# Performance work log

Measured on AMD Instinct MI355X. Metric: run time of the kernel, lower is better.

The kernel has to match this reference:

```python
import jax, jax.numpy as jnp
import numpy as np

NUM_SCENES = 7
SHAPE = [512, 512, 256, 64]  # layer dims: 512->512->256->64
BATCH = 16384


def _xavier(key, shape):
    # nn.init.xavier_normal_ on (s, in, out): fan_in/fan_out from last two dims
    fan_in, fan_out = shape[-2], shape[-1]
    std = np.sqrt(2.0 / (fan_in + fan_out)).astype(np.float32)
    return jax.random.normal(key, shape, dtype=jnp.float32) * std


def setup_inputs() -> dict:
    key = jax.random.key(0)
    ks = jax.random.split(key, 16)
    inp = {
        "x": jax.random.normal(ks[0], (BATCH, SHAPE[0]), dtype=jnp.float32),
        "scene": jax.random.randint(ks[1], (BATCH,), 1, NUM_SCENES + 1, dtype=jnp.int64),
    }
    for i in range(3):
        din, dout = SHAPE[i], SHAPE[i + 1]
        inp[f"W{i}"] = _xavier(ks[2 + 4 * i], (NUM_SCENES, din, dout))
        inp[f"b{i}"] = jnp.zeros((NUM_SCENES, dout), dtype=jnp.float32)
        inp[f"gW{i}"] = _xavier(ks[3 + 4 * i], (1, din, dout))
        inp[f"gb{i}"] = jnp.zeros((1, dout), dtype=jnp.float32)
    return inp


def _star_linear(x, scene0, W, b, gW, gb, relu):
    # W: (S, in, out), gW: (1, in, out). Equivalent to gathering W[scene0]
    # and doing x[:,None,:] @ (w * gW), but computed as a dense GEMM over
    # all scenes followed by a per-sample select (avoids B*in*out gather).
    scaled = W * gW                                   # (S, in, out)
    out_all = jnp.einsum('bi,sio->bso', x, scaled)    # (B, S, out)
    out = jnp.take_along_axis(out_all, scene0[:, None, None], axis=1)[:, 0, :]
    out = out + b[scene0] + gb[0]
    if relu:
        out = jnp.maximum(out, 0.0)
    return out  # dropout is identity at eval


def reference(x, scene, W0, b0, gW0, gb0, W1, b1, gW1, gb1, W2, b2, gW2, gb2):
    scene0 = (scene - 1).astype(jnp.int32)
    h = _star_linear(x, scene0, W0, b0, gW0, gb0, relu=True)
    h = _star_linear(h, scene0, W1, b1, gW1, gb1, relu=True)
    h = _star_linear(h, scene0, W2, b2, gW2, gb2, relu=False)  # drop=True -> no relu
    return h
```

## Files before the change

### kernel.cpp

```cpp
#include <hip/hip_runtime.h>
#include <hip/hip_bf16.h>
#include <stdint.h>


#define BATCH   16384
#define NSCENE  7
#define TM      128
#define NBLK    (BATCH / 256)
#define MT_MAX  (BATCH / TM + NSCENE)
#define PADMAX  (BATCH + NSCENE * TM)

typedef __bf16 bf16x8 __attribute__((ext_vector_type(8)));
typedef float  f32x4  __attribute__((ext_vector_type(4)));

__device__ __forceinline__ ushort f2bf(float f) {
  union { float f; uint32_t u; } v; v.f = f;
  uint32_t r = (v.u + 0x7FFFu + ((v.u >> 16) & 1u)) >> 16;
  return (ushort)r;
}
__device__ __forceinline__ uint32_t pk2(float a, float b) {
  union { __hip_bfloat162 h; uint32_t u; } cv;
  cv.h = __float22bfloat162_rn(make_float2(a, b));
  return cv.u;
}
__device__ __forceinline__ void async16(const void* g, void* lds) {
  __builtin_amdgcn_global_load_lds(
      (const __attribute__((address_space(1))) uint32_t*)g,
      (__attribute__((address_space(3))) uint32_t*)lds, 16, 0, 0);
}

__device__ __forceinline__ void st_tile64(const float* __restrict__ W,
                                          const float* __restrict__ gW,
                                          ushort* __restrict__ sT,
                                          int K, int N, int s, int n0, int k0,
                                          int tid, float (*tl)[65]) {
  int tx = tid & 15, ty = tid >> 4;
  const float* Wp = W + (size_t)s * K * N;
#pragma unroll
  for (int i = 0; i < 4; i++) {
    int k = k0 + ty + i * 16;
    const float4 w = *(const float4*)&Wp[(size_t)k * N + n0 + tx * 4];
    const float4 g = *(const float4*)&gW[(size_t)k * N + n0 + tx * 4];
    float* row = &tl[ty + i * 16][tx * 4];
    row[0] = w.x * g.x; row[1] = w.y * g.y;
    row[2] = w.z * g.z; row[3] = w.w * g.w;
  }
  __syncthreads();
  int n_l = tid >> 2, kq = tid & 3;
  uint4 u0, u1;
  u0.x = pk2(tl[kq * 16 + 0][n_l],  tl[kq * 16 + 1][n_l]);
  u0.y = pk2(tl[kq * 16 + 2][n_l],  tl[kq * 16 + 3][n_l]);
  u0.z = pk2(tl[kq * 16 + 4][n_l],  tl[kq * 16 + 5][n_l]);
  u0.w = pk2(tl[kq * 16 + 6][n_l],  tl[kq * 16 + 7][n_l]);
  u1.x = pk2(tl[kq * 16 + 8][n_l],  tl[kq * 16 + 9][n_l]);
  u1.y = pk2(tl[kq * 16 + 10][n_l], tl[kq * 16 + 11][n_l]);
  u1.z = pk2(tl[kq * 16 + 12][n_l], tl[kq * 16 + 13][n_l]);
  u1.w = pk2(tl[kq * 16 + 14][n_l], tl[kq * 16 + 15][n_l]);
  uint4* dst = (uint4*)&sT[((size_t)s * N + n0 + n_l) * K + k0 + kq * 16];
  dst[0] = u0; dst[1] = u1;
}

#define NB_W0 (8 * 8 * 7)
#define NB_W1 (4 * 8 * 7)
#define NB_W2 (1 * 4 * 7)
#define NB_BIAS 23
#define NB_CNT NBLK

__global__ __launch_bounds__(256) void prep_k(
    const float* __restrict__ W0, const float* __restrict__ gW0,
    const float* __restrict__ W1, const float* __restrict__ gW1,
    const float* __restrict__ W2, const float* __restrict__ gW2,
    const float* __restrict__ b0, const float* __restrict__ gb0,
    const float* __restrict__ b1, const float* __restrict__ gb1,
    const float* __restrict__ b2, const float* __restrict__ gb2,
    const int* __restrict__ scene,
    ushort* __restrict__ sT0, ushort* __restrict__ sT1, ushort* __restrict__ sT2,
    float* __restrict__ bias0, float* __restrict__ bias1, float* __restrict__ bias2,
    int* __restrict__ bcnt, int* __restrict__ rank) {
  __shared__ float tl[64][65];
  int bid = blockIdx.x, tid = threadIdx.x;
  if (bid < NB_W0) {
    int l = bid, r = l % 64;
    st_tile64(W0, gW0, sT0, 512, 512, l / 64, (r % 8) * 64, (r / 8) * 64, tid, tl);
  } else if (bid < NB_W0 + NB_W1) {
    int l = bid - NB_W0, r = l % 32;
    st_tile64(W1, gW1, sT1, 512, 256, l / 32, (r % 4) * 64, (r / 4) * 64, tid, tl);
  } else if (bid < NB_W0 + NB_W1 + NB_W2) {
    int l = bid - NB_W0 - NB_W1;
    st_tile64(W2, gW2, sT2, 256, 64, l / 4, 0, (l % 4) * 64, tid, tl);
  } else if (bid < NB_W0 + NB_W1 + NB_W2 + NB_BIAS) {
    int t = (bid - NB_W0 - NB_W1 - NB_W2) * 256 + tid;
    if (t < 7 * 512) bias0[t] = b0[t] + gb0[t & 511];
    else if (t < 7 * 512 + 7 * 256) { int i = t - 7 * 512; bias1[i] = b1[i] + gb1[i & 255]; }
    else if (t < 7 * 512 + 7 * 256 + 7 * 64) { int i = t - 7 * 512 - 7 * 256; bias2[i] = b2[i] + gb2[i & 63]; }
  } else {
    __shared__ int l[NSCENE];
    if (tid < NSCENE) l[tid] = 0;
    __syncthreads();
    int blk = bid - NB_W0 - NB_W1 - NB_W2 - NB_BIAS;
    int i = blk * 256 + tid;
    int pos = atomicAdd(&l[scene[i] - 1], 1);
    rank[i] = pos;
    __syncthreads();
    if (tid < NSCENE) bcnt[blk * NSCENE + tid] = l[tid];
  }
}

__global__ __launch_bounds__(256) void xc_k(const float* __restrict__ x,
                                            const int* __restrict__ scene,
                                            const int* __restrict__ rank,
                                            const int* __restrict__ bcnt,
                                            int* __restrict__ idxp,
                                            ushort* __restrict__ xc,
                                            int* __restrict__ plan_g,
                                            float* __restrict__ out) {
  __shared__ int sb[NBLK * NSCENE];
  __shared__ int tot[NSCENE], padoff[NSCENE], cumt[NSCENE + 1];
  __shared__ int pre[NSCENE], base7[NSCENE];
  int tid = threadIdx.x;
  ((float2*)out)[(size_t)blockIdx.x * 256 + tid] = make_float2(0.f, 0.f);
  if (tid < NBLK * NSCENE) sb[tid] = bcnt[tid];
  if (tid + 256 < NBLK * NSCENE) sb[tid + 256] = bcnt[tid + 256];
  __syncthreads();
  int myblk = blockIdx.x >> 5;
  if (tid < 224) {
    int s = tid >> 5, l = tid & 31;
    int a0 = sb[l * NSCENE + s], a1 = sb[(l + 32) * NSCENE + s];
    int all = a0 + a1;
    int msk = (l < myblk ? a0 : 0) + (l + 32 < myblk ? a1 : 0);
#pragma unroll
    for (int m = 16; m >= 1; m >>= 1) {
      all += __shfl_xor(all, m, 32);
      msk += __shfl_xor(msk, m, 32);
    }
    if (l == 0) { tot[s] = all; pre[s] = msk; }
  }
  __syncthreads();
  if (tid == 0) {
    int po = 0, ct = 0;
#pragma unroll
    for (int s = 0; s < NSCENE; s++) {
      padoff[s] = po; cumt[s] = ct;
      int tiles = (tot[s] + TM - 1) / TM;
      ct += tiles; po += tiles * TM;
    }
    cumt[NSCENE] = ct;
  }
  __syncthreads();
  if (tid < NSCENE) base7[tid] = padoff[tid] + pre[tid];
  if (blockIdx.x == 0) {
    if (tid < NSCENE) { plan_g[tid] = tot[tid]; plan_g[7 + tid] = padoff[tid]; }
    if (tid < NSCENE + 1) plan_g[14 + tid] = cumt[tid];
  }
  __syncthreads();

  int r = blockIdx.x * 8 + (tid >> 5);
  int s = scene[r] - 1;
  int d = base7[s] + rank[r];
  if ((tid & 31) == 0) idxp[d] = r;
  int c = (tid & 31) * 16;
  const float4* p = (const float4*)(x + (size_t)r * 512 + c);
  float4 f0 = p[0], f1 = p[1], f2 = p[2], f3 = p[3];
  uint4 v0, v1;
  v0.x = pk2(f0.x, f0.y); v0.y = pk2(f0.z, f0.w);
  v0.z = pk2(f1.x, f1.y); v0.w = pk2(f1.z, f1.w);
  v1.x = pk2(f2.x, f2.y); v1.y = pk2(f2.z, f2.w);
  v1.z = pk2(f3.x, f3.y); v1.w = pk2(f3.z, f3.w);
  uint4* q = (uint4*)(xc + (size_t)d * 512 + c);
  q[0] = v0; q[1] = v1;
}

__global__ __launch_bounds__(256) void gemm0_k(
    const ushort* __restrict__ ain, const ushort* __restrict__ bw,
    const float* __restrict__ bias, const int* __restrict__ plan,
    ushort* __restrict__ hout) {
  __shared__ int splan[24];
  __shared__ __align__(16) ushort Abuf[64 * 64];
  __shared__ __align__(16) ushort Bbuf[128 * 64];

  int tid = threadIdx.x;
  if (tid < 22) splan[tid] = plan[tid];
  __syncthreads();
  const int* padoff = splan + 7;
  const int* cumt   = splan + 14;

  int j = blockIdx.x;
  int t = j >> 1;
  if (t >= cumt[NSCENE]) return;
  int sc = 0;
  while (sc < NSCENE - 1 && t >= cumt[sc + 1]) sc++;
  int mrow0 = padoff[sc] + (t - cumt[sc]) * TM + (j & 1) * 64;
  int nb = blockIdx.y;

  int lane = tid & 63, wid = tid >> 6;

  f32x4 acc[4][2];
#pragma unroll
  for (int mt = 0; mt < 4; mt++)
#pragma unroll
    for (int nt = 0; nt < 2; nt++) acc[mt][nt] = (f32x4){0.f, 0.f, 0.f, 0.f};

  const ushort* bwS = bw + ((size_t)sc * 512 + (size_t)nb * 128) * 512;

  for (int kb = 0; kb < 8; kb++) {
#pragma unroll
    for (int i = 0; i < 2; i++) {
      int c = tid + i * 256;
      int row = c >> 3, q = c & 7;
      int kg = q ^ (row & 7);
      async16(ain + (size_t)(mrow0 + row) * 512 + kb * 64 + kg * 8,
              &Abuf[(size_t)(i * 256 + wid * 64) * 8]);
    }
#pragma unroll
    for (int i = 0; i < 4; i++) {
      int c = tid + i * 256;
      int row = c >> 3, q = c & 7;
      int kg = q ^ (row & 7);
      async16(bwS + (size_t)row * 512 + kb * 64 + kg * 8,
              &Bbuf[(size_t)(i * 256 + wid * 64) * 8]);
    }
    __syncthreads();
#pragma unroll
    for (int kk = 0; kk < 64; kk += 32) {
      bf16x8 af[4], bfr[2];
      int kc = (kk >> 3) + (lane >> 4);
#pragma unroll
      for (int mt = 0; mt < 4; mt++) {
        int row = mt * 16 + (lane & 15);
        af[mt] = *(const bf16x8*)(&Abuf[(row * 8 + (kc ^ (row & 7))) * 8]);
      }
#pragma unroll
      for (int nt = 0; nt < 2; nt++) {
        int row = wid * 32 + nt * 16 + (lane & 15);
        bfr[nt] = *(const bf16x8*)(&Bbuf[(row * 8 + (kc ^ (row & 7))) * 8]);
      }
#pragma unroll
      for (int mt = 0; mt < 4; mt++)
#pragma unroll
        for (int nt = 0; nt < 2; nt++)
          acc[mt][nt] = __builtin_amdgcn_mfma_f32_16x16x32_bf16(af[mt], bfr[nt], acc[mt][nt], 0, 0, 0);
    }
    __syncthreads();
  }

#pragma unroll
  for (int mt = 0; mt < 4; mt++) {
    int rl0 = mt * 16 + (lane >> 4) * 4;
#pragma unroll
    for (int nt = 0; nt < 2; nt++) {
      int col = nb * 128 + wid * 32 + nt * 16 + (lane & 15);
      float bv = bias[sc * 512 + col];
#pragma unroll
      for (int r = 0; r < 4; r++) {
        float v = fmaxf(acc[mt][nt][r] + bv, 0.f);
        hout[(size_t)(mrow0 + rl0 + r) * 512 + col] = f2bf(v);
      }
    }
  }
}

__global__ __launch_bounds__(256) void gemm1_k(
    const ushort* __restrict__ hc1, const ushort* __restrict__ sT1,
    const ushort* __restrict__ sT2, const float* __restrict__ bias1,
    const float* __restrict__ bias2, const int* __restrict__ plan,
    const int* __restrict__ idxp, float* __restrict__ out) {
  __shared__ int splan[24];
  __shared__ __align__(16) ushort Abuf[64 * 64];
  __shared__ __align__(16) ushort Bbuf[128 * 64];
  __shared__ __align__(16) ushort h2[64 * 128];

  int tid = threadIdx.x;
  if (tid < 22) splan[tid] = plan[tid];
  __syncthreads();
  const int* tot    = splan;
  const int* padoff = splan + 7;
  const int* cumt   = splan + 14;

  int j = blockIdx.x;
  int t = j >> 1;
  if (t >= cumt[NSCENE]) return;
  int sc = 0;
  while (sc < NSCENE - 1 && t >= cumt[sc + 1]) sc++;
  int mrow0 = padoff[sc] + (t - cumt[sc]) * TM + (j & 1) * 64;
  int maxloc = padoff[sc] + tot[sc];
  if (mrow0 >= maxloc) return;
  int kr = blockIdx.y;

  int lane = tid & 63, wid = tid >> 6;

  f32x4 acc[4][2];
#pragma unroll
  for (int mt = 0; mt < 4; mt++)
#pragma unroll
    for (int nt = 0; nt < 2; nt++) acc[mt][nt] = (f32x4){0.f, 0.f, 0.f, 0.f};

  const ushort* b1p = sT1 + ((size_t)sc * 256 + (size_t)kr * 128) * 512;

  for (int kb = 0; kb < 8; kb++) {
#pragma unroll
    for (int i = 0; i < 2; i++) {
      int c = tid + i * 256;
      int row = c >> 3, q = c & 7;
      int kg = q ^ (row & 7);
      async16(hc1 + (size_t)(mrow0 + row) * 512 + kb * 64 + kg * 8,
              &Abuf[(size_t)(i * 256 + wid * 64) * 8]);
    }
#pragma unroll
    for (int i = 0; i < 4; i++) {
      int c = tid + i * 256;
      int row = c >> 3, q = c & 7;
      int kg = q ^ (row & 7);
      async16(b1p + (size_t)row * 512 + kb * 64 + kg * 8,
              &Bbuf[(size_t)(i * 256 + wid * 64) * 8]);
    }
    __syncthreads();
#pragma unroll
    for (int kk = 0; kk < 64; kk += 32) {
      bf16x8 af[4], bfr[2];
      int kc = (kk >> 3) + (lane >> 4);
#pragma unroll
      for (int mt = 0; mt < 4; mt++) {
        int row = mt * 16 + (lane & 15);
        af[mt] = *(const bf16x8*)(&Abuf[(row * 8 + (kc ^ (row & 7))) * 8]);
      }
#pragma unroll
      for (int nt = 0; nt < 2; nt++) {
        int row = wid * 32 + nt * 16 + (lane & 15);
        bfr[nt] = *(const bf16x8*)(&Bbuf[(row * 8 + (kc ^ (row & 7))) * 8]);
      }
#pragma unroll
      for (int mt = 0; mt < 4; mt++)
#pragma unroll
        for (int nt = 0; nt < 2; nt++)
          acc[mt][nt] = __builtin_amdgcn_mfma_f32_16x16x32_bf16(af[mt], bfr[nt], acc[mt][nt], 0, 0, 0);
    }
    __syncthreads();
  }

#pragma unroll
  for (int mt = 0; mt < 4; mt++) {
#pragma unroll
    for (int nt = 0; nt < 2; nt++) {
      int col = wid * 32 + nt * 16 + (lane & 15);
      float bv = bias1[sc * 256 + kr * 128 + col];
#pragma unroll
      for (int r = 0; r < 4; r++) {
        int row = mt * 16 + (lane >> 4) * 4 + r;
        float v = fmaxf(acc[mt][nt][r] + bv, 0.f);
        int cc = col >> 3;
        int cs = (cc & 8) | ((cc & 7) ^ (row & 7));
        h2[(row * 16 + cs) * 8 + (col & 7)] = f2bf(v);
      }
    }
  }
  __syncthreads();

  const ushort* b2p = sT2 + (size_t)sc * 64 * 256 + (size_t)kr * 128;
#pragma unroll
  for (int i = 0; i < 4; i++) {
    int p = tid + i * 256;
    int row = p >> 4, q = p & 15;
    int kg = (q & 8) | ((q & 7) ^ (row & 7));
    async16(b2p + (size_t)row * 256 + kg * 8,
            &Bbuf[(size_t)(i * 256 + wid * 64) * 8]);
  }
  __syncthreads();

  f32x4 acc2[4];
#pragma unroll
  for (int nt = 0; nt < 4; nt++) acc2[nt] = (f32x4){0.f, 0.f, 0.f, 0.f};

#pragma unroll
  for (int kk = 0; kk < 128; kk += 32) {
    int kc = (kk >> 3) + (lane >> 4);
    bf16x8 af;
    {
      int row = wid * 16 + (lane & 15);
      int ks = (kc & 8) | ((kc & 7) ^ (row & 7));
      af = *(const bf16x8*)(&h2[(row * 16 + ks) * 8]);
    }
    bf16x8 bfr[4];
#pragma unroll
    for (int nt = 0; nt < 4; nt++) {
      int n = nt * 16 + (lane & 15);
      int ks = (kc & 8) | ((kc & 7) ^ (n & 7));
      bfr[nt] = *(const bf16x8*)(&Bbuf[(n * 16 + ks) * 8]);
    }
#pragma unroll
    for (int nt = 0; nt < 4; nt++)
      acc2[nt] = __builtin_amdgcn_mfma_f32_16x16x32_bf16(af, bfr[nt], acc2[nt], 0, 0, 0);
  }

  int rowg[4], gidx[4];
#pragma unroll
  for (int r = 0; r < 4; r++) {
    rowg[r] = mrow0 + wid * 16 + (lane >> 4) * 4 + r;
    gidx[r] = idxp[rowg[r]];
  }
#pragma unroll
  for (int nt = 0; nt < 4; nt++) {
    int col = nt * 16 + (lane & 15);
    float bv = (kr == 0) ? bias2[sc * 64 + col] : 0.f;
#pragma unroll
    for (int r = 0; r < 4; r++) {
      if (rowg[r] < maxloc)
        atomicAdd(&out[(size_t)gidx[r] * 64 + col], acc2[nt][r] + bv);
    }
  }
}

extern "C" void kernel_launch(void* const* d_in, const int* in_sizes, int n_in,
                              void* d_out, int out_size, void* d_ws, size_t ws_size,
                              hipStream_t stream) {
  const float* x   = (const float*)d_in[0];
  const int* scene = (const int*)d_in[1];
  const float* W0  = (const float*)d_in[2];
  const float* b0  = (const float*)d_in[3];
  const float* gW0 = (const float*)d_in[4];
  const float* gb0 = (const float*)d_in[5];
  const float* W1  = (const float*)d_in[6];
  const float* b1  = (const float*)d_in[7];
  const float* gW1 = (const float*)d_in[8];
  const float* gb1 = (const float*)d_in[9];
  const float* W2  = (const float*)d_in[10];
  const float* b2  = (const float*)d_in[11];
  const float* gW2 = (const float*)d_in[12];
  const float* gb2 = (const float*)d_in[13];
  float* out = (float*)d_out;

  char* ws = (char*)d_ws;
  size_t off = 0;
  auto alloc = [&](size_t bytes) -> void* {
    void* p = ws + off;
    off = (off + bytes + 255) & ~(size_t)255;
    return p;
  };
  ushort* sT0   = (ushort*)alloc((size_t)7 * 512 * 512 * 2);
  ushort* sT1   = (ushort*)alloc((size_t)7 * 256 * 512 * 2);
  ushort* sT2   = (ushort*)alloc((size_t)7 * 64 * 256 * 2);
  float*  bias0 = (float*)alloc(7 * 512 * 4);
  float*  bias1 = (float*)alloc(7 * 256 * 4);
  float*  bias2 = (float*)alloc(7 * 64 * 4);
  int*    bcnt  = (int*)alloc(NBLK * NSCENE * 4);
  int*    rank  = (int*)alloc(BATCH * 4);
  int*    idxp  = (int*)alloc(PADMAX * 4);
  int*    plan  = (int*)alloc(32 * 4);
  ushort* xc    = (ushort*)alloc((size_t)PADMAX * 512 * 2);
  ushort* hc1   = (ushort*)alloc((size_t)PADMAX * 512 * 2);
  (void)ws_size; (void)n_in; (void)in_sizes; (void)out_size;

  prep_k<<<NB_W0 + NB_W1 + NB_W2 + NB_BIAS + NB_CNT, 256, 0, stream>>>(
      W0, gW0, W1, gW1, W2, gW2, b0, gb0, b1, gb1, b2, gb2, scene,
      sT0, sT1, sT2, bias0, bias1, bias2, bcnt, rank);
  xc_k<<<BATCH / 8, 256, 0, stream>>>(x, scene, rank, bcnt, idxp, xc, plan, out);

  gemm0_k<<<dim3(MT_MAX * 2, 4), 256, 0, stream>>>(xc, sT0, bias0, plan, hc1);
  gemm1_k<<<dim3(MT_MAX * 2, 2), 256, 0, stream>>>(hc1, sT1, sT2, bias1, bias2,
                                                   plan, idxp, out);
}
```

Measured before the change: 150.1 us.

## Split scene counting into its own kernel and fuse weight prep with x compaction

Scene counting moves out of the prep kernel into a small standalone count kernel. Weight scaling/transposition, bias merging and x compaction/bf16 conversion are merged into one launch. The weight-prep blocks and the x-compaction blocks now run concurrently instead of back to back, because only the counting has to come first. The kernel count stays the same, but the combined kernel uses more shared memory per block, which may reduce occupancy.

```diff
diff --git a/kernel.cpp b/kernel.cpp
--- a/kernel.cpp
+++ b/kernel.cpp
@@ -27,6 +27,20 @@
   __builtin_amdgcn_global_load_lds(
       (const __attribute__((address_space(1))) uint32_t*)g,
       (__attribute__((address_space(3))) uint32_t*)lds, 16, 0, 0);
+}
+
+__global__ __launch_bounds__(256) void count_k(const int* __restrict__ scene,
+                                               int* __restrict__ bcnt,
+                                               int* __restrict__ rank) {
+  __shared__ int l[NSCENE];
+  int tid = threadIdx.x, blk = blockIdx.x;
+  if (tid < NSCENE) l[tid] = 0;
+  __syncthreads();
+  int i = blk * 256 + tid;
+  int pos = atomicAdd(&l[scene[i] - 1], 1);
+  rank[i] = pos;
+  __syncthreads();
+  if (tid < NSCENE) bcnt[blk * NSCENE + tid] = l[tid];
 }
 
 __device__ __forceinline__ void st_tile64(const float* __restrict__ W,
@@ -64,65 +78,51 @@
 #define NB_W1 (4 * 8 * 7)
 #define NB_W2 (1 * 4 * 7)
 #define NB_BIAS 23
-#define NB_CNT NBLK
-
-__global__ __launch_bounds__(256) void prep_k(
+#define NB_XC  (BATCH / 8)
+
+__global__ __launch_bounds__(256) void prepxc_k(
     const float* __restrict__ W0, const float* __restrict__ gW0,
     const float* __restrict__ W1, const float* __restrict__ gW1,
     const float* __restrict__ W2, const float* __restrict__ gW2,
     const float* __restrict__ b0, const float* __restrict__ gb0,
     const float* __restrict__ b1, const float* __restrict__ gb1,
     const float* __restrict__ b2, const float* __restrict__ gb2,
-    const int* __restrict__ scene,
+    const float* __restrict__ x, const int* __restrict__ scene,
+    const int* __restrict__ rank, const int* __restrict__ bcnt,
     ushort* __restrict__ sT0, ushort* __restrict__ sT1, ushort* __restrict__ sT2,
     float* __restrict__ bias0, float* __restrict__ bias1, float* __restrict__ bias2,
-    int* __restrict__ bcnt, int* __restrict__ rank) {
+    int* __restrict__ idxp, ushort* __restrict__ xc,
+    int* __restrict__ plan_g, float* __restrict__ out) {
   __shared__ float tl[64][65];
+  __shared__ int sb[NBLK * NSCENE];
+  __shared__ int tot[NSCENE], padoff[NSCENE], cumt[NSCENE + 1];
+  __shared__ int pre[NSCENE], base7[NSCENE];
   int bid = blockIdx.x, tid = threadIdx.x;
   if (bid < NB_W0) {
     int l = bid, r = l % 64;
     st_tile64(W0, gW0, sT0, 512, 512, l / 64, (r % 8) * 64, (r / 8) * 64, tid, tl);
+    return;
   } else if (bid < NB_W0 + NB_W1) {
     int l = bid - NB_W0, r = l % 32;
     st_tile64(W1, gW1, sT1, 512, 256, l / 32, (r % 4) * 64, (r / 4) * 64, tid, tl);
+    return;
   } else if (bid < NB_W0 + NB_W1 + NB_W2) {
     int l = bid - NB_W0 - NB_W1;
     st_tile64(W2, gW2, sT2, 256, 64, l / 4, 0, (l % 4) * 64, tid, tl);
+    return;
   } else if (bid < NB_W0 + NB_W1 + NB_W2 + NB_BIAS) {
     int t = (bid - NB_W0 - NB_W1 - NB_W2) * 256 + tid;
     if (t < 7 * 512) bias0[t] = b0[t] + gb0[t & 511];
     else if (t < 7 * 512 + 7 * 256) { int i = t - 7 * 512; bias1[i] = b1[i] + gb1[i & 255]; }
     else if (t < 7 * 512 + 7 * 256 + 7 * 64) { int i = t - 7 * 512 - 7 * 256; bias2[i] = b2[i] + gb2[i & 63]; }
-  } else {
-    __shared__ int l[NSCENE];
-    if (tid < NSCENE) l[tid] = 0;
-    __syncthreads();
-    int blk = bid - NB_W0 - NB_W1 - NB_W2 - NB_BIAS;
-    int i = blk * 256 + tid;
-    int pos = atomicAdd(&l[scene[i] - 1], 1);
-    rank[i] = pos;
-    __syncthreads();
-    if (tid < NSCENE) bcnt[blk * NSCENE + tid] = l[tid];
-  }
-}
-
-__global__ __launch_bounds__(256) void xc_k(const float* __restrict__ x,
-                                            const int* __restrict__ scene,
-                                            const int* __restrict__ rank,
-                                            const int* __restrict__ bcnt,
-                                            int* __restrict__ idxp,
-                                            ushort* __restrict__ xc,
-                                            int* __restrict__ plan_g,
-                                            float* __restrict__ out) {
-  __shared__ int sb[NBLK * NSCENE];
-  __shared__ int tot[NSCENE], padoff[NSCENE], cumt[NSCENE + 1];
-  __shared__ int pre[NSCENE], base7[NSCENE];
-  int tid = threadIdx.x;
-  ((float2*)out)[(size_t)blockIdx.x * 256 + tid] = make_float2(0.f, 0.f);
+    return;
+  }
+  int xb = bid - (NB_W0 + NB_W1 + NB_W2 + NB_BIAS);
+  ((float2*)out)[(size_t)xb * 256 + tid] = make_float2(0.f, 0.f);
   if (tid < NBLK * NSCENE) sb[tid] = bcnt[tid];
   if (tid + 256 < NBLK * NSCENE) sb[tid + 256] = bcnt[tid + 256];
   __syncthreads();
-  int myblk = blockIdx.x >> 5;
+  int myblk = xb >> 5;
   if (tid < 224) {
     int s = tid >> 5, l = tid & 31;
     int a0 = sb[l * NSCENE + s], a1 = sb[(l + 32) * NSCENE + s];
@@ -148,13 +148,13 @@
   }
   __syncthreads();
   if (tid < NSCENE) base7[tid] = padoff[tid] + pre[tid];
-  if (blockIdx.x == 0) {
+  if (xb == 0) {
     if (tid < NSCENE) { plan_g[tid] = tot[tid]; plan_g[7 + tid] = padoff[tid]; }
     if (tid < NSCENE + 1) plan_g[14 + tid] = cumt[tid];
   }
   __syncthreads();
 
-  int r = blockIdx.x * 8 + (tid >> 5);
+  int r = xb * 8 + (tid >> 5);
   int s = scene[r] - 1;
   int d = base7[s] + rank[r];
   if ((tid & 31) == 0) idxp[d] = r;
@@ -449,10 +449,10 @@
   ushort* hc1   = (ushort*)alloc((size_t)PADMAX * 512 * 2);
   (void)ws_size; (void)n_in; (void)in_sizes; (void)out_size;
 
-  prep_k<<<NB_W0 + NB_W1 + NB_W2 + NB_BIAS + NB_CNT, 256, 0, stream>>>(
-      W0, gW0, W1, gW1, W2, gW2, b0, gb0, b1, gb1, b2, gb2, scene,
-      sT0, sT1, sT2, bias0, bias1, bias2, bcnt, rank);
-  xc_k<<<BATCH / 8, 256, 0, stream>>>(x, scene, rank, bcnt, idxp, xc, plan, out);
+  count_k<<<NBLK, 256, 0, stream>>>(scene, bcnt, rank);
+  prepxc_k<<<NB_W0 + NB_W1 + NB_W2 + NB_BIAS + NB_XC, 256, 0, stream>>>(
+      W0, gW0, W1, gW1, W2, gW2, b0, gb0, b1, gb1, b2, gb2, x, scene,
+      rank, bcnt, sT0, sT1, sT2, bias0, bias1, bias2, idxp, xc, plan, out);
 
   gemm0_k<<<dim3(MT_MAX * 2, 4), 256, 0, stream>>>(xc, sT0, bias0, plan, hc1);
   gemm1_k<<<dim3(MT_MAX * 2, 2), 256, 0, stream>>>(hc1, sT1, sT2, bias1, bias2,
```

Measured after the change: 152.5 us. About the same (+1.6%).
